# Kernel optimization log

Measured on AMD Instinct MI355X. Metric: run time of the kernel, lower is better.

## Reference

```python
import jax, jax.numpy as jnp
import numpy as np

D_MODEL = 1024
NUM_HEADS = 16
HEAD_DIM = D_MODEL // NUM_HEADS


def setup_inputs() -> dict:
    key = jax.random.key(0)
    ks = jax.random.split(key, 11)
    B, S, D = 2, 2048, D_MODEL
    scale = 1.0 / np.sqrt(D)
    inp = {
        "q": jax.random.normal(ks[0], (B, S, D), dtype=jnp.float32),
        "k": jax.random.normal(ks[1], (B, S, D), dtype=jnp.float32),
        "v": jax.random.normal(ks[2], (B, S, D), dtype=jnp.float32),
        # torch nn.Linear weights are [out, in]; y = x @ W.T + b
        "Wq": jax.random.normal(ks[3], (D, D), dtype=jnp.float32) * scale,
        "bq": jnp.zeros((D,), dtype=jnp.float32),
        "Wk": jax.random.normal(ks[4], (D, D), dtype=jnp.float32) * scale,
        "bk": jnp.zeros((D,), dtype=jnp.float32),
        "Wv": jax.random.normal(ks[5], (D, D), dtype=jnp.float32) * scale,
        "bv": jnp.zeros((D,), dtype=jnp.float32),
        "Wo": jax.random.normal(ks[6], (D, D), dtype=jnp.float32) * scale,
        "bo": jnp.zeros((D,), dtype=jnp.float32),
    }
    return inp


def _split_heads(x):
    B, S, D = x.shape
    return x.reshape(B, S, NUM_HEADS, HEAD_DIM).transpose(0, 2, 1, 3)  # [B,H,S,hd]


def reference(q, k, v, Wq, bq, Wk, bk, Wv, bv, Wo, bo):
    B, S, D = q.shape
    qh = _split_heads(q @ Wq.T + bq)
    kh = _split_heads(k @ Wk.T + bk)
    vh = _split_heads(v @ Wv.T + bv)
    # scores: [B,H,S,S], causal mask, softmax
    scores = jnp.einsum("bhqd,bhkd->bhqk", qh, kh) / jnp.sqrt(
        jnp.asarray(HEAD_DIM, dtype=qh.dtype))
    causal = jnp.tril(jnp.ones((S, S), dtype=bool))
    scores = jnp.where(causal[None, None], scores, -jnp.inf)
    attn = jax.nn.softmax(scores, axis=-1)
    out = jnp.einsum("bhqk,bhkd->bhqd", attn, vh)  # [B,H,S,hd]
    out = out.transpose(0, 2, 1, 3).reshape(B, S, D)
    return out @ Wo.T + bo
```

## Files before the change

### kernel.cpp

```cpp
#include <hip/hip_runtime.h>
#include <hip/hip_bf16.h>
#include <cstdint>
#include <cstddef>

typedef __bf16 bf16;
typedef __bf16 bf16x2 __attribute__((ext_vector_type(2)));
typedef __bf16 bf16x4 __attribute__((ext_vector_type(4)));
typedef __bf16 bf16x8 __attribute__((ext_vector_type(8)));
typedef float f32x4 __attribute__((ext_vector_type(4)));
typedef float f32x16 __attribute__((ext_vector_type(16)));
typedef unsigned int u32x4 __attribute__((ext_vector_type(4)));

#define S_LEN 2048
#define DM 1024
#define NH 16
#define HD 64
#define NQKV (4096 * 1024)
#define NW (1024 * 1024)
#define QK_SCALE 0.18033688011112042f

__device__ __forceinline__ void gload_lds16(const bf16* g, bf16* l) {
  __builtin_amdgcn_global_load_lds(
      (const __attribute__((address_space(1))) void*)g,
      (__attribute__((address_space(3))) void*)l, 16, 0, 0);
}

__device__ __forceinline__ unsigned packbf(float lo, float hi) {
  bf16x2 t;
  t[0] = (bf16)lo;
  t[1] = (bf16)hi;
  return __builtin_bit_cast(unsigned, t);
}

__device__ __forceinline__ void pl32swap(unsigned& a, unsigned& b) {
#if __has_builtin(__builtin_amdgcn_permlane32_swap)
  auto r = __builtin_amdgcn_permlane32_swap((int)a, (int)b, false, false);
  a = (unsigned)r[0];
  b = (unsigned)r[1];
#else
  asm volatile("v_permlane32_swap_b32 %0, %1" : "+v"(a), "+v"(b));
#endif
}

__global__ __launch_bounds__(256) void cvt_all(
    const float* __restrict__ q, const float* __restrict__ k, const float* __restrict__ v,
    const float* __restrict__ Wq, const float* __restrict__ Wk, const float* __restrict__ Wv,
    const float* __restrict__ Wo, bf16* __restrict__ out) {
  const size_t i = ((size_t)blockIdx.x * 256 + threadIdx.x) * 8;
  const float* src;
  size_t off;
  if (i < (size_t)NQKV) { src = q; off = i; }
  else if (i < 2ull * NQKV) { src = k; off = i - NQKV; }
  else if (i < 3ull * NQKV) { src = v; off = i - 2ull * NQKV; }
  else {
    const size_t j = i - 3ull * NQKV;
    if (j < (size_t)NW) { src = Wq; off = j; }
    else if (j < 2ull * NW) { src = Wk; off = j - NW; }
    else if (j < 3ull * NW) { src = Wv; off = j - 2ull * NW; }
    else { src = Wo; off = j - 3ull * NW; }
  }
  const float4 a = *(const float4*)(src + off);
  const float4 b = *(const float4*)(src + off + 4);
  bf16x8 o;
  o[0] = (bf16)a.x; o[1] = (bf16)a.y; o[2] = (bf16)a.z; o[3] = (bf16)a.w;
  o[4] = (bf16)b.x; o[5] = (bf16)b.y; o[6] = (bf16)b.z; o[7] = (bf16)b.w;
  *(bf16x8*)(out + i) = o;
}

template <int MODE>
__global__ __launch_bounds__(256, 2) void gemm_bt(
    const bf16* __restrict__ A, const bf16* __restrict__ W,
    const float* __restrict__ bias0, const float* __restrict__ bias1,
    const float* __restrict__ bias2, void* __restrict__ Out,
    int M, int N, int K, float scale) {
  __shared__ __align__(16) bf16 sm[2 * 128 * 64];
  bf16* Asl = sm;
  bf16* Bsl = sm + 128 * 64;
  const int tid = threadIdx.x;
  const int lane = tid & 63, w = tid >> 6;
  const int wr = w >> 1, wc = w & 1;
  const int r16 = lane & 15, grp = lane >> 4;

  int flat = blockIdx.y * gridDim.x + blockIdx.x;
  const int cpx = (gridDim.x * gridDim.y) >> 3;
  flat = (flat & 7) * cpx + (flat >> 3);
  const int m0 = (flat / gridDim.x) * 128;
  const int n0 = (flat % gridDim.x) * 128;

  const int seg = n0 >> 10;
  const bf16* Ab = (MODE == 3) ? A + (size_t)seg * NQKV : A;

  f32x4 acc[4][4] = {};

  const int nk = K >> 6;
  for (int t = 0; t < nk; ++t) {
    const int k0 = t << 6;
    __syncthreads();
#pragma unroll
    for (int j = 0; j < 4; ++j) {
      const int lin = j * 256 + tid;
      const int rr = lin >> 3;
      const int cc = (lin & 7) * 8;
      gload_lds16(&Ab[(size_t)(m0 + rr) * K + k0 + cc], &Asl[lin * 8]);
      gload_lds16(&W[(size_t)(n0 + rr) * K + k0 + cc], &Bsl[lin * 8]);
    }
    __syncthreads();
#pragma unroll
    for (int kk = 0; kk < 2; ++kk) {
      bf16x8 af[4], bfr[4];
#pragma unroll
      for (int m = 0; m < 4; ++m)
        af[m] = *(const bf16x8*)&Asl[(wr * 64 + m * 16 + r16) * 64 + kk * 32 + grp * 8];
#pragma unroll
      for (int n = 0; n < 4; ++n)
        bfr[n] = *(const bf16x8*)&Bsl[(wc * 64 + n * 16 + r16) * 64 + kk * 32 + grp * 8];
#pragma unroll
      for (int m = 0; m < 4; ++m)
#pragma unroll
        for (int n = 0; n < 4; ++n)
          acc[m][n] = __builtin_amdgcn_mfma_f32_16x16x32_bf16(af[m], bfr[n], acc[m][n], 0, 0, 0);
    }
  }

  const float* bp = (MODE == 3) ? (seg == 0 ? bias0 : (seg == 1 ? bias1 : bias2)) : bias0;
  const float sc = (MODE == 3) ? (seg == 0 ? scale : 1.0f) : scale;

  if (MODE == 3 && seg == 2) {
    __syncthreads();
    bf16* T = sm + w * (32 * 76);
    const int b = (m0 + wr * 64) >> 11;
    const int srow0 = (m0 + wr * 64) & 2047;
    bf16* base2 = (bf16*)Out + 2 * (size_t)NQKV;
#pragma unroll
    for (int p = 0; p < 2; ++p) {
#pragma unroll
      for (int nn = 0; nn < 2; ++nn) {
        const int n = 2 * p + nn;
#pragma unroll
        for (int mq = 0; mq < 4; ++mq)
#pragma unroll
          for (int r = 0; r < 4; ++r) {
            const int d_l = nn * 16 + r16;
            const int s_l = mq * 16 + grp * 4 + r;
            const int cs = (n0 + wc * 64 + n * 16 + r16) & 1023;
            T[d_l * 76 + s_l] = (bf16)(acc[mq][n][r] + bp[cs]);
          }
      }
      __syncthreads();
#pragma unroll
      for (int j = 0; j < 4; ++j) {
        const int d_l = j * 8 + (lane >> 3);
        const int scnk = lane & 7;
        const uint2 lo = *(const uint2*)&T[d_l * 76 + scnk * 8];
        const uint2 hi = *(const uint2*)&T[d_l * 76 + scnk * 8 + 4];
        const int cs = (n0 + wc * 64 + p * 32 + d_l) & 1023;
        const int hh = cs >> 6, dd = cs & 63;
        bf16* dst = base2 + ((size_t)(b * NH + hh) * HD + dd) * S_LEN + srow0 + scnk * 8;
        uint4 val; val.x = lo.x; val.y = lo.y; val.z = hi.x; val.w = hi.y;
        *(uint4*)dst = val;
      }
      __syncthreads();
    }
    return;
  }

#pragma unroll
  for (int m = 0; m < 4; ++m) {
#pragma unroll
    for (int n = 0; n < 4; ++n) {
#pragma unroll
      for (int r = 0; r < 4; ++r) {
        const int row = m0 + wr * 64 + m * 16 + grp * 4 + r;
        const int col = n0 + wc * 64 + n * 16 + r16;
        const int cs = col & 1023;
        const float v = (acc[m][n][r] + bp[cs]) * sc;
        if (MODE == 3) {
          const int b = row >> 11, s = row & 2047, h = cs >> 6, d = cs & 63;
          bf16* base = (bf16*)Out + (size_t)seg * NQKV;
          base[((size_t)(b * NH + h) * S_LEN + s) * HD + d] = (bf16)v;
        } else {
          ((float*)Out)[(size_t)row * N + col] = v;
        }
      }
    }
  }
}

__global__ __launch_bounds__(128, 2) void attn_fwd5(
    const bf16* __restrict__ Qh, const bf16* __restrict__ Kh,
    const bf16* __restrict__ Vt, bf16* __restrict__ AO) {
  __shared__ __align__(16) bf16 Kl[2][64 * 64];
  __shared__ __align__(16) bf16 Vl[2][64 * 64];

  const int tid = threadIdx.x;
  const int lane = tid & 63, w = tid >> 6;
  const int q31 = lane & 31, h = lane >> 5;

  const int bid = blockIdx.x;
  const int xcd = bid & 7;
  const int idx = bid >> 3;
  const int cc = 31 - (idx >> 2);
  const int bh = xcd * 4 + (idx & 3);
  const int q0 = cc * 64;
  const int nt = cc + 1;
  const int q0w = q0 + 32 * w;
  const int qg = q0w + q31;

  const bf16* Qb = Qh + (size_t)bh * S_LEN * HD;
  const bf16* Kb = Kh + (size_t)bh * S_LEN * HD;
  const bf16* Vb = Vt + (size_t)bh * HD * S_LEN;

  int stK[4], stV[4], stL[4];
#pragma unroll
  for (int i = 0; i < 4; ++i) {
    const int lin = i * 128 + tid;
    const int row = lin >> 3;
    const int colb = (lin & 7) * 16;
    const int scol = colb ^ ((row & 7) << 4);
    stK[i] = row * HD + (scol >> 1);
    stV[i] = row * S_LEN + (scol >> 1);
    stL[i] = lin * 8;
  }

  bf16x8 qf[4];
#pragma unroll
  for (int ks = 0; ks < 4; ++ks)
    qf[ks] = *(const bf16x8*)&Qb[(size_t)qg * HD + ks * 16 + 8 * h];

  f32x16 accO[2] = {};
  float m = -1e30f, l = 0.f;

  const int swz = (q31 & 7) << 4;

#pragma unroll
  for (int i = 0; i < 4; ++i) {
    gload_lds16(&Kb[stK[i]], &Kl[0][stL[i]]);
    gload_lds16(&Vb[stV[i]], &Vl[0][stL[i]]);
  }
  __syncthreads();

  int cur = 0;
  for (int kt = 0; kt < nt; ++kt) {
    const int k0 = kt << 6;
    if (kt + 1 < nt) {
      const int kn = (kt + 1) << 6;
      bf16* kd = Kl[cur ^ 1];
      bf16* vd = Vl[cur ^ 1];
#pragma unroll
      for (int i = 0; i < 4; ++i) {
        gload_lds16(&Kb[(size_t)kn * HD + stK[i]], &kd[stL[i]]);
        gload_lds16(&Vb[kn + stV[i]], &vd[stL[i]]);
      }
    }

    const bf16* KlC = Kl[cur];
    const bf16* VlC = Vl[cur];
    const bool diag = (kt == nt - 1);
    const bool skip1 = diag && (w == 0);

    bf16x8 kf[8];
#pragma unroll
    for (int ks = 0; ks < 4; ++ks) {
      const int c = (32 * ks + 16 * h) ^ swz;
      kf[ks]     = *(const bf16x8*)((const char*)KlC + q31 * 128 + c);
      kf[4 + ks] = *(const bf16x8*)((const char*)KlC + (32 + q31) * 128 + c);
    }

    f32x16 p0 = {}, p1 = {};
    __builtin_amdgcn_s_setprio(1);
#pragma unroll
    for (int ks = 0; ks < 4; ++ks)
      p0 = __builtin_amdgcn_mfma_f32_32x32x16_bf16(kf[ks], qf[ks], p0, 0, 0, 0);
    __builtin_amdgcn_s_setprio(0);
    if (!skip1) {
      __builtin_amdgcn_s_setprio(1);
#pragma unroll
      for (int ks = 0; ks < 4; ++ks)
        p1 = __builtin_amdgcn_mfma_f32_32x32x16_bf16(kf[4 + ks], qf[ks], p1, 0, 0, 0);
      __builtin_amdgcn_s_setprio(0);
    } else {
#pragma unroll
      for (int r = 0; r < 16; ++r) p1[r] = -1e30f;
    }

    bf16x8 vf01[4];
#pragma unroll
    for (int ks = 0; ks < 2; ++ks)
#pragma unroll
      for (int db = 0; db < 2; ++db) {
        const int c = (32 * ks + 16 * h) ^ swz;
        vf01[ks * 2 + db] =
            *(const bf16x8*)((const char*)VlC + (db * 32 + q31) * 128 + c);
      }

    if (diag) {
#pragma unroll
      for (int r = 0; r < 16; ++r) {
        const int key = k0 + (r & 3) + 8 * (r >> 2) + 4 * h;
        if (key > qg) p0[r] = -1e30f;
        if (!skip1 && key + 32 > qg) p1[r] = -1e30f;
      }
    }
    float t[16];
#pragma unroll
    for (int r = 0; r < 16; ++r) t[r] = fmaxf(p0[r], p1[r]);
#pragma unroll
    for (int s = 8; s >= 1; s >>= 1)
#pragma unroll
      for (int r = 0; r < s; ++r) t[r] = fmaxf(t[r], t[r + s]);
    const float pmax = fmaxf(t[0], __shfl_xor(t[0], 32));
    if (!__all(pmax - m <= 8.0f)) {
      const float mn = fmaxf(m, pmax);
      const float alpha = exp2f(m - mn);
      m = mn;
      l *= alpha;
#pragma unroll
      for (int r = 0; r < 16; ++r) { accO[0][r] *= alpha; accO[1][r] *= alpha; }
    }
    float smv[16];
#pragma unroll
    for (int r = 0; r < 16; ++r) {
      p0[r] = exp2f(p0[r] - m);
      p1[r] = exp2f(p1[r] - m);
      smv[r] = p0[r] + p1[r];
    }
#pragma unroll
    for (int s = 8; s >= 1; s >>= 1)
#pragma unroll
      for (int r = 0; r < s; ++r) smv[r] += smv[r + s];
    l += smv[0] + __shfl_xor(smv[0], 32);

    unsigned pw[4][4];
#define PACK_HALF(P, o0, o1)                                                   \
  {                                                                            \
    unsigned wv[8];                                                            \
    _Pragma("unroll") for (int mm = 0; mm < 8; ++mm)                           \
        wv[mm] = packbf(P[2 * mm], P[2 * mm + 1]);                             \
    pl32swap(wv[0], wv[2]);                                                    \
    pl32swap(wv[1], wv[3]);                                                    \
    pl32swap(wv[4], wv[6]);                                                    \
    pl32swap(wv[5], wv[7]);                                                    \
    pw[o0][0] = wv[0]; pw[o0][1] = wv[1]; pw[o0][2] = wv[2]; pw[o0][3] = wv[3];\
    pw[o1][0] = wv[4]; pw[o1][1] = wv[5]; pw[o1][2] = wv[6]; pw[o1][3] = wv[7];\
  }
    PACK_HALF(p0, 0, 1)
    if (!skip1) PACK_HALF(p1, 2, 3)
#undef PACK_HALF

    bf16x8 vf23[4];
    if (!skip1) {
#pragma unroll
      for (int ks = 2; ks < 4; ++ks)
#pragma unroll
        for (int db = 0; db < 2; ++db) {
          const int c = (32 * ks + 16 * h) ^ swz;
          vf23[(ks - 2) * 2 + db] =
              *(const bf16x8*)((const char*)VlC + (db * 32 + q31) * 128 + c);
        }
    }

#define PV_STEP(ks, vfa)                                                       \
  {                                                                            \
    u32x4 pu = {pw[ks][0], pw[ks][1], pw[ks][2], pw[ks][3]};                   \
    const bf16x8 pf_ = __builtin_bit_cast(bf16x8, pu);                         \
    accO[0] = __builtin_amdgcn_mfma_f32_32x32x16_bf16(vfa[(ks & 1) * 2 + 0],   \
                                                      pf_, accO[0], 0, 0, 0);  \
    accO[1] = __builtin_amdgcn_mfma_f32_32x32x16_bf16(vfa[(ks & 1) * 2 + 1],   \
                                                      pf_, accO[1], 0, 0, 0);  \
  }
    __builtin_amdgcn_s_setprio(1);
    PV_STEP(0, vf01)
    PV_STEP(1, vf01)
    __builtin_amdgcn_s_setprio(0);
    if (!skip1) {
      __builtin_amdgcn_s_setprio(1);
      PV_STEP(2, vf23)
      PV_STEP(3, vf23)
      __builtin_amdgcn_s_setprio(0);
    }
#undef PV_STEP

    __syncthreads();
    cur ^= 1;
  }

  const float ro = 1.0f / l;
  const int b = bh >> 4, hh = bh & 15;
  bf16* orow = AO + ((size_t)(b * S_LEN + qg)) * DM + hh * HD;
#pragma unroll
  for (int db = 0; db < 2; ++db) {
#pragma unroll
    for (int mm = 0; mm < 4; ++mm) {
      bf16x4 ov;
#pragma unroll
      for (int t = 0; t < 4; ++t) ov[t] = (bf16)(accO[db][4 * mm + t] * ro);
      *(bf16x4*)&orow[db * 32 + 8 * mm + 4 * h] = ov;
    }
  }
}

extern "C" void kernel_launch(void* const* d_in, const int* in_sizes, int n_in,
                              void* d_out, int out_size, void* d_ws, size_t ws_size,
                              hipStream_t stream) {
  const float* q  = (const float*)d_in[0];
  const float* k  = (const float*)d_in[1];
  const float* v  = (const float*)d_in[2];
  const float* Wq = (const float*)d_in[3];
  const float* bq = (const float*)d_in[4];
  const float* bk = (const float*)d_in[6];
  const float* bv = (const float*)d_in[8];
  const float* Wo = (const float*)d_in[9];
  const float* bo = (const float*)d_in[10];

  const int NTOK = 2 * S_LEN;

  bf16* qb  = (bf16*)d_ws;
  bf16* Wqb = qb + 3 * (size_t)NQKV;
  bf16* Wob = Wqb + 3 * (size_t)NW;
  bf16* Qh  = Wqb + 4 * (size_t)NW;
  bf16* Kh  = Qh + (size_t)NQKV;
  bf16* Vt  = Kh + (size_t)NQKV;
  bf16* AO  = Vt + (size_t)NQKV;

  const int cvt_blocks = (3 * NQKV + 4 * NW) / 8 / 256;
  cvt_all<<<cvt_blocks, 256, 0, stream>>>(q, k, (const float*)d_in[2],
                                          (const float*)d_in[3], (const float*)d_in[5],
                                          (const float*)d_in[7], Wo, qb);

  gemm_bt<3><<<dim3(3 * DM / 128, NTOK / 128), 256, 0, stream>>>(
      qb, Wqb, bq, bk, bv, Qh, NTOK, 3 * DM, DM, QK_SCALE);

  attn_fwd5<<<dim3(1024), 128, 0, stream>>>(Qh, Kh, Vt, AO);

  gemm_bt<2><<<dim3(DM / 128, NTOK / 128), 256, 0, stream>>>(
      AO, Wob, bo, bo, bo, d_out, NTOK, DM, DM, 1.0f);
}
```

Measured before the change: 135.7 us.

## Enlarge attention tiles to 128 queries with triple-buffered K/V and balanced ordering

The attention kernel now runs 4 waves per block covering 128 query rows instead of 64, so each K/V tile loaded into LDS is shared by twice as many waves. K/V loading moves from double to triple buffering, using explicit vmcnt waits and a single barrier per iteration. Blocks are ordered so light and heavy causal rows are paired, and each wave skips tiles beyond its own causal limit. This costs more LDS per block and adds wait/barrier complexity, and waves on the diagonal sit idle while the block's other waves finish.

```diff
diff --git a/kernel.cpp b/kernel.cpp
--- a/kernel.cpp
+++ b/kernel.cpp
@@ -186,11 +186,11 @@
   }
 }
 
-__global__ __launch_bounds__(128, 2) void attn_fwd5(
+__global__ __launch_bounds__(256, 2) void attn_fwd6(
     const bf16* __restrict__ Qh, const bf16* __restrict__ Kh,
     const bf16* __restrict__ Vt, bf16* __restrict__ AO) {
-  __shared__ __align__(16) bf16 Kl[2][64 * 64];
-  __shared__ __align__(16) bf16 Vl[2][64 * 64];
+  __shared__ __align__(16) bf16 Kl[3][64 * 64];
+  __shared__ __align__(16) bf16 Vl[3][64 * 64];
 
   const int tid = threadIdx.x;
   const int lane = tid & 63, w = tid >> 6;
@@ -198,22 +198,23 @@
 
   const int bid = blockIdx.x;
   const int xcd = bid & 7;
-  const int idx = bid >> 3;
-  const int cc = 31 - (idx >> 2);
-  const int bh = xcd * 4 + (idx & 3);
-  const int q0 = cc * 64;
-  const int nt = cc + 1;
+  const int within = bid >> 3;
+  const int bh = xcd * 4 + (within >> 4);
+  const int cc = (within < 32) ? 15 - (within & 15) : (within & 15);
+  const int q0 = cc * 128;
+  const int nt = 2 * cc + 2;
   const int q0w = q0 + 32 * w;
+  const int nt_w = (q0w >> 6) + 1;
   const int qg = q0w + q31;
 
   const bf16* Qb = Qh + (size_t)bh * S_LEN * HD;
   const bf16* Kb = Kh + (size_t)bh * S_LEN * HD;
   const bf16* Vb = Vt + (size_t)bh * HD * S_LEN;
 
-  int stK[4], stV[4], stL[4];
-#pragma unroll
-  for (int i = 0; i < 4; ++i) {
-    const int lin = i * 128 + tid;
+  int stK[2], stV[2], stL[2];
+#pragma unroll
+  for (int i = 0; i < 2; ++i) {
+    const int lin = i * 256 + tid;
     const int row = lin >> 3;
     const int colb = (lin & 7) * 16;
     const int scol = colb ^ ((row & 7) << 4);
@@ -229,108 +230,125 @@
 
   f32x16 accO[2] = {};
   float m = -1e30f, l = 0.f;
-
   const int swz = (q31 & 7) << 4;
 
 #pragma unroll
-  for (int i = 0; i < 4; ++i) {
+  for (int i = 0; i < 2; ++i) {
     gload_lds16(&Kb[stK[i]], &Kl[0][stL[i]]);
     gload_lds16(&Vb[stV[i]], &Vl[0][stL[i]]);
   }
-  __syncthreads();
+  if (nt > 1) {
+#pragma unroll
+    for (int i = 0; i < 2; ++i) {
+      gload_lds16(&Kb[(size_t)64 * HD + stK[i]], &Kl[1][stL[i]]);
+      gload_lds16(&Vb[64 + stV[i]], &Vl[1][stL[i]]);
+    }
+  }
 
   int cur = 0;
   for (int kt = 0; kt < nt; ++kt) {
-    const int k0 = kt << 6;
-    if (kt + 1 < nt) {
-      const int kn = (kt + 1) << 6;
-      bf16* kd = Kl[cur ^ 1];
-      bf16* vd = Vl[cur ^ 1];
-#pragma unroll
-      for (int i = 0; i < 4; ++i) {
+    if (kt + 1 < nt) asm volatile("s_waitcnt vmcnt(4)" ::: "memory");
+    else             asm volatile("s_waitcnt vmcnt(0)" ::: "memory");
+    __builtin_amdgcn_s_barrier();
+
+    if (kt + 2 < nt) {
+      int nxt = cur + 2; if (nxt >= 3) nxt -= 3;
+      const int kn = (kt + 2) << 6;
+      bf16* kd = Kl[nxt];
+      bf16* vd = Vl[nxt];
+#pragma unroll
+      for (int i = 0; i < 2; ++i) {
         gload_lds16(&Kb[(size_t)kn * HD + stK[i]], &kd[stL[i]]);
         gload_lds16(&Vb[kn + stV[i]], &vd[stL[i]]);
       }
     }
 
-    const bf16* KlC = Kl[cur];
-    const bf16* VlC = Vl[cur];
-    const bool diag = (kt == nt - 1);
-    const bool skip1 = diag && (w == 0);
-
-    bf16x8 kf[8];
-#pragma unroll
-    for (int ks = 0; ks < 4; ++ks) {
-      const int c = (32 * ks + 16 * h) ^ swz;
-      kf[ks]     = *(const bf16x8*)((const char*)KlC + q31 * 128 + c);
-      kf[4 + ks] = *(const bf16x8*)((const char*)KlC + (32 + q31) * 128 + c);
-    }
-
-    f32x16 p0 = {}, p1 = {};
-    __builtin_amdgcn_s_setprio(1);
-#pragma unroll
-    for (int ks = 0; ks < 4; ++ks)
-      p0 = __builtin_amdgcn_mfma_f32_32x32x16_bf16(kf[ks], qf[ks], p0, 0, 0, 0);
-    __builtin_amdgcn_s_setprio(0);
-    if (!skip1) {
+    if (kt < nt_w) {
+      const int k0 = kt << 6;
+      const bf16* KlC = Kl[cur];
+      const bf16* VlC = Vl[cur];
+      const bool diag = (kt == nt_w - 1);
+      const bool skip1 = diag && (k0 + 32 > q0w + 31);
+
+      bf16x8 kf[8];
+#pragma unroll
+      for (int ks = 0; ks < 4; ++ks) {
+        const int c = (32 * ks + 16 * h) ^ swz;
+        kf[ks] = *(const bf16x8*)((const char*)KlC + q31 * 128 + c);
+      }
+      if (!skip1) {
+#pragma unroll
+        for (int ks = 0; ks < 4; ++ks) {
+          const int c = (32 * ks + 16 * h) ^ swz;
+          kf[4 + ks] = *(const bf16x8*)((const char*)KlC + (32 + q31) * 128 + c);
+        }
+      }
+
+      f32x16 p0 = {}, p1 = {};
       __builtin_amdgcn_s_setprio(1);
 #pragma unroll
       for (int ks = 0; ks < 4; ++ks)
-        p1 = __builtin_amdgcn_mfma_f32_32x32x16_bf16(kf[4 + ks], qf[ks], p1, 0, 0, 0);
+        p0 = __builtin_amdgcn_mfma_f32_32x32x16_bf16(kf[ks], qf[ks], p0, 0, 0, 0);
       __builtin_amdgcn_s_setprio(0);
-    } else {
-#pragma unroll
-      for (int r = 0; r < 16; ++r) p1[r] = -1e30f;
-    }
-
-    bf16x8 vf01[4];
-#pragma unroll
-    for (int ks = 0; ks < 2; ++ks)
-#pragma unroll
-      for (int db = 0; db < 2; ++db) {
-        const int c = (32 * ks + 16 * h) ^ swz;
-        vf01[ks * 2 + db] =
-            *(const bf16x8*)((const char*)VlC + (db * 32 + q31) * 128 + c);
-      }
-
-    if (diag) {
+      if (!skip1) {
+        __builtin_amdgcn_s_setprio(1);
+#pragma unroll
+        for (int ks = 0; ks < 4; ++ks)
+          p1 = __builtin_amdgcn_mfma_f32_32x32x16_bf16(kf[4 + ks], qf[ks], p1, 0, 0, 0);
+        __builtin_amdgcn_s_setprio(0);
+      } else {
+#pragma unroll
+        for (int r = 0; r < 16; ++r) p1[r] = -1e30f;
+      }
+
+      bf16x8 vf01[4];
+#pragma unroll
+      for (int ks = 0; ks < 2; ++ks)
+#pragma unroll
+        for (int db = 0; db < 2; ++db) {
+          const int c = (32 * ks + 16 * h) ^ swz;
+          vf01[ks * 2 + db] =
+              *(const bf16x8*)((const char*)VlC + (db * 32 + q31) * 128 + c);
+        }
+
+      if (diag) {
+#pragma unroll
+        for (int r = 0; r < 16; ++r) {
+          const int key = k0 + (r & 3) + 8 * (r >> 2) + 4 * h;
+          if (key > qg) p0[r] = -1e30f;
+          if (!skip1 && key + 32 > qg) p1[r] = -1e30f;
+        }
+      }
+      float t[16];
+#pragma unroll
+      for (int r = 0; r < 16; ++r) t[r] = fmaxf(p0[r], p1[r]);
+#pragma unroll
+      for (int s = 8; s >= 1; s >>= 1)
+#pragma unroll
+        for (int r = 0; r < s; ++r) t[r] = fmaxf(t[r], t[r + s]);
+      const float pmax = fmaxf(t[0], __shfl_xor(t[0], 32));
+      if (!__all(pmax - m <= 8.0f)) {
+        const float mn = fmaxf(m, pmax);
+        const float alpha = exp2f(m - mn);
+        m = mn;
+        l *= alpha;
+#pragma unroll
+        for (int r = 0; r < 16; ++r) { accO[0][r] *= alpha; accO[1][r] *= alpha; }
+      }
+      float smv[16];
 #pragma unroll
       for (int r = 0; r < 16; ++r) {
-        const int key = k0 + (r & 3) + 8 * (r >> 2) + 4 * h;
-        if (key > qg) p0[r] = -1e30f;
-        if (!skip1 && key + 32 > qg) p1[r] = -1e30f;
-      }
-    }
-    float t[16];
-#pragma unroll
-    for (int r = 0; r < 16; ++r) t[r] = fmaxf(p0[r], p1[r]);
-#pragma unroll
-    for (int s = 8; s >= 1; s >>= 1)
-#pragma unroll
-      for (int r = 0; r < s; ++r) t[r] = fmaxf(t[r], t[r + s]);
-    const float pmax = fmaxf(t[0], __shfl_xor(t[0], 32));
-    if (!__all(pmax - m <= 8.0f)) {
-      const float mn = fmaxf(m, pmax);
-      const float alpha = exp2f(m - mn);
-      m = mn;
-      l *= alpha;
-#pragma unroll
-      for (int r = 0; r < 16; ++r) { accO[0][r] *= alpha; accO[1][r] *= alpha; }
-    }
-    float smv[16];
-#pragma unroll
-    for (int r = 0; r < 16; ++r) {
-      p0[r] = exp2f(p0[r] - m);
-      p1[r] = exp2f(p1[r] - m);
-      smv[r] = p0[r] + p1[r];
-    }
-#pragma unroll
-    for (int s = 8; s >= 1; s >>= 1)
-#pragma unroll
-      for (int r = 0; r < s; ++r) smv[r] += smv[r + s];
-    l += smv[0] + __shfl_xor(smv[0], 32);
-
-    unsigned pw[4][4];
+        p0[r] = exp2f(p0[r] - m);
+        p1[r] = exp2f(p1[r] - m);
+        smv[r] = p0[r] + p1[r];
+      }
+#pragma unroll
+      for (int s = 8; s >= 1; s >>= 1)
+#pragma unroll
+        for (int r = 0; r < s; ++r) smv[r] += smv[r + s];
+      l += smv[0] + __shfl_xor(smv[0], 32);
+
+      unsigned pw[4][4];
 #define PACK_HALF(P, o0, o1)                                                   \
   {                                                                            \
     unsigned wv[8];                                                            \
@@ -343,21 +361,21 @@
     pw[o0][0] = wv[0]; pw[o0][1] = wv[1]; pw[o0][2] = wv[2]; pw[o0][3] = wv[3];\
     pw[o1][0] = wv[4]; pw[o1][1] = wv[5]; pw[o1][2] = wv[6]; pw[o1][3] = wv[7];\
   }
-    PACK_HALF(p0, 0, 1)
-    if (!skip1) PACK_HALF(p1, 2, 3)
+      PACK_HALF(p0, 0, 1)
+      if (!skip1) PACK_HALF(p1, 2, 3)
 #undef PACK_HALF
 
-    bf16x8 vf23[4];
-    if (!skip1) {
-#pragma unroll
-      for (int ks = 2; ks < 4; ++ks)
-#pragma unroll
-        for (int db = 0; db < 2; ++db) {
-          const int c = (32 * ks + 16 * h) ^ swz;
-          vf23[(ks - 2) * 2 + db] =
-              *(const bf16x8*)((const char*)VlC + (db * 32 + q31) * 128 + c);
-        }
-    }
+      bf16x8 vf23[4];
+      if (!skip1) {
+#pragma unroll
+        for (int ks = 2; ks < 4; ++ks)
+#pragma unroll
+          for (int db = 0; db < 2; ++db) {
+            const int c = (32 * ks + 16 * h) ^ swz;
+            vf23[(ks - 2) * 2 + db] =
+                *(const bf16x8*)((const char*)VlC + (db * 32 + q31) * 128 + c);
+          }
+      }
 
 #define PV_STEP(ks, vfa)                                                       \
   {                                                                            \
@@ -368,20 +386,20 @@
     accO[1] = __builtin_amdgcn_mfma_f32_32x32x16_bf16(vfa[(ks & 1) * 2 + 1],   \
                                                       pf_, accO[1], 0, 0, 0);  \
   }
-    __builtin_amdgcn_s_setprio(1);
-    PV_STEP(0, vf01)
-    PV_STEP(1, vf01)
-    __builtin_amdgcn_s_setprio(0);
-    if (!skip1) {
       __builtin_amdgcn_s_setprio(1);
-      PV_STEP(2, vf23)
-      PV_STEP(3, vf23)
+      PV_STEP(0, vf01)
+      PV_STEP(1, vf01)
       __builtin_amdgcn_s_setprio(0);
-    }
+      if (!skip1) {
+        __builtin_amdgcn_s_setprio(1);
+        PV_STEP(2, vf23)
+        PV_STEP(3, vf23)
+        __builtin_amdgcn_s_setprio(0);
+      }
 #undef PV_STEP
-
-    __syncthreads();
-    cur ^= 1;
+    }
+
+    ++cur; if (cur == 3) cur = 0;
   }
 
   const float ro = 1.0f / l;
@@ -407,7 +425,9 @@
   const float* v  = (const float*)d_in[2];
   const float* Wq = (const float*)d_in[3];
   const float* bq = (const float*)d_in[4];
+  const float* Wk = (const float*)d_in[5];
   const float* bk = (const float*)d_in[6];
+  const float* Wv = (const float*)d_in[7];
   const float* bv = (const float*)d_in[8];
   const float* Wo = (const float*)d_in[9];
   const float* bo = (const float*)d_in[10];
@@ -423,14 +443,12 @@
   bf16* AO  = Vt + (size_t)NQKV;
 
   const int cvt_blocks = (3 * NQKV + 4 * NW) / 8 / 256;
-  cvt_all<<<cvt_blocks, 256, 0, stream>>>(q, k, (const float*)d_in[2],
-                                          (const float*)d_in[3], (const float*)d_in[5],
-                                          (const float*)d_in[7], Wo, qb);
+  cvt_all<<<cvt_blocks, 256, 0, stream>>>(q, k, v, Wq, Wk, Wv, Wo, qb);
 
   gemm_bt<3><<<dim3(3 * DM / 128, NTOK / 128), 256, 0, stream>>>(
       qb, Wqb, bq, bk, bv, Qh, NTOK, 3 * DM, DM, QK_SCALE);
 
-  attn_fwd5<<<dim3(1024), 128, 0, stream>>>(Qh, Kh, Vt, AO);
+  attn_fwd6<<<dim3(512), 256, 0, stream>>>(Qh, Kh, Vt, AO);
 
   gemm_bt<2><<<dim3(DM / 128, NTOK / 128), 256, 0, stream>>>(
       AO, Wob, bo, bo, bo, d_out, NTOK, DM, DM, 1.0f);
```

Result: no change. 133.2 us (-1.8%).
